# Kernel tuning notes

Hardware: AMD Instinct MI355X
Metric: run time of the kernel (lower is better)

Reference implementation:

```python
import jax, jax.numpy as jnp
import numpy as np

NUM_HEADS = 16
KEY_SIZE = 64
MODEL = NUM_HEADS * KEY_SIZE
B, S = 4, 2048
NEG = jnp.float32(-1e9)


def alibi_bidirectional_bias(num_heads, seq_len):
    # slopes for num_heads//2 heads: 1 / x**(i+1), x = 24**(1/h)
    h = num_heads // 2
    x = 24.0 ** (1.0 / h)
    slopes = (1.0 / x ** jnp.arange(1, h + 1, dtype=jnp.float32))[:, None, None]  # [h,1,1]
    i = jnp.arange(seq_len)
    rel = (i[None, :] - i[:, None]).astype(jnp.float32)  # rel[i,j] = j - i
    # forward (causal): tril(j - i) + (-1e9 strictly above diag)
    fwd = slopes * jnp.tril(rel) + jnp.triu(jnp.full((seq_len, seq_len), NEG), k=1)
    # backward (anti-causal): triu(i - j) + (-1e9 strictly below diag)
    bwd = slopes * jnp.triu(-rel) + jnp.tril(jnp.full((seq_len, seq_len), NEG), k=-1)
    return jnp.concatenate([fwd, bwd], axis=0)  # [num_heads, S, S]


def setup_inputs() -> dict:
    key = jax.random.key(0)
    ks = jax.random.split(key, 11)
    sc = 0.02
    d = {
        "query": jax.random.normal(ks[0], (B, S, MODEL), jnp.float32),
        "key": jax.random.normal(ks[1], (B, S, MODEL), jnp.float32),
        "value": jax.random.normal(ks[2], (B, S, MODEL), jnp.float32),
        "Wq": jax.random.normal(ks[3], (MODEL, MODEL), jnp.float32) * sc,
        "bq": jnp.zeros((MODEL,), jnp.float32),
        "Wk": jax.random.normal(ks[4], (MODEL, MODEL), jnp.float32) * sc,
        "bk": jnp.zeros((MODEL,), jnp.float32),
        "Wv": jax.random.normal(ks[5], (MODEL, MODEL), jnp.float32) * sc,
        "bv": jnp.zeros((MODEL,), jnp.float32),
        "Wo": jax.random.normal(ks[6], (MODEL, MODEL), jnp.float32) * sc,
        "bo": jnp.zeros((MODEL,), jnp.float32),
    }
    return d


def reference(query, key, value, Wq, bq, Wk, bk, Wv, bv, Wo, bo):
    b, s, _ = query.shape
    H, D = NUM_HEADS, KEY_SIZE

    def proj(x, W, bias):
        return (x @ W.T + bias).reshape(b, s, H, D).transpose(0, 2, 1, 3)  # [B,H,S,D]

    q = proj(query, Wq, bq)
    k = proj(key, Wk, bk)
    v = proj(value, Wv, bv)

    bias = alibi_bidirectional_bias(H, s)  # [H,S,S], broadcasts over batch
    scores = jnp.einsum("bhqd,bhkd->bhqk", q, k) / jnp.sqrt(jnp.float32(D)) + bias
    attn = jax.nn.softmax(scores, axis=-1)
    out = jnp.einsum("bhqk,bhkd->bhqd", attn, v)
    out = out.transpose(0, 2, 1, 3).reshape(b, s, H * D)
    return out @ Wo.T + bo
```

## Files before the change

kernel.cpp:

```cpp
#include <hip/hip_runtime.h>
#include <hip/hip_bf16.h>
#include <stdint.h>

typedef unsigned short u16;
typedef __attribute__((ext_vector_type(8))) __bf16 bf16x8;
typedef __attribute__((ext_vector_type(4))) float f32x4;
typedef __attribute__((ext_vector_type(4))) unsigned int u32x4;

#define S_LEN 2048
#define NHEAD 16
#define HDIM 64
#define DMODEL 1024
#define NBATCH 4
#define MTOK (NBATCH * S_LEN)

__device__ __forceinline__ u16 f2bf(float f) {
    uint32_t u = __float_as_uint(f);
    u += 0x7fffu + ((u >> 16) & 1u);
    return (u16)(u >> 16);
}

__device__ __forceinline__ void gld_lds16(const u16* g, u16* l) {
    __builtin_amdgcn_global_load_lds(
        (const __attribute__((address_space(1))) void*)g,
        (__attribute__((address_space(3))) void*)l, 16, 0, 0);
}

__global__ __launch_bounds__(256) void cast_all(
        const float* __restrict__ q, const float* __restrict__ k, const float* __restrict__ v,
        const float* __restrict__ wq, const float* __restrict__ wk,
        const float* __restrict__ wv, const float* __restrict__ wo,
        u16* __restrict__ xq, u16* __restrict__ xk, u16* __restrict__ xv,
        u16* __restrict__ wqb, u16* __restrict__ wkb, u16* __restrict__ wvb,
        u16* __restrict__ wob) {
    size_t idx4 = (size_t)blockIdx.x * 256 + threadIdx.x;
    const float* src;
    u16* dst;
    size_t off;
    if (idx4 < (size_t)3 << 21) {
        int t = (int)(idx4 >> 21);
        off = (idx4 & ((1u << 21) - 1)) * 4;
        src = (t == 0) ? q : (t == 1) ? k : v;
        dst = (t == 0) ? xq : (t == 1) ? xk : xv;
    } else {
        size_t w = idx4 - ((size_t)3 << 21);
        int t = (int)(w >> 18);
        off = (w & ((1u << 18) - 1)) * 4;
        src = (t == 0) ? wq : (t == 1) ? wk : (t == 2) ? wv : wo;
        dst = (t == 0) ? wqb : (t == 1) ? wkb : (t == 2) ? wvb : wob;
    }
    float4 val = *(const float4*)(src + off);
    ushort4 o;
    o.x = f2bf(val.x); o.y = f2bf(val.y); o.z = f2bf(val.z); o.w = f2bf(val.w);
    *(ushort4*)(dst + off) = o;
}

#define TM 128
#define TN 128

__device__ __forceinline__ void gemm_body(const u16* __restrict__ A,
                                          const u16* __restrict__ W,
                                          const float* __restrict__ bias,
                                          void* __restrict__ outp, int mode,
                                          int m0, int n0) {
    __shared__ __align__(16) u16 As[2][TM * 32];
    __shared__ __align__(16) u16 Bs[2][TN * 32];
    const int tid  = threadIdx.x;
    const int lane = tid & 63;
    const int wv   = tid >> 6;
    const int l16  = lane & 15;
    const int quad = lane >> 4;
    const int wm   = (wv >> 1) * 64;
    const int wn   = (wv & 1) * 64;

    f32x4 acc[4][4];
#pragma unroll
    for (int i = 0; i < 4; i++)
#pragma unroll
        for (int j = 0; j < 4; j++) acc[i][j] = {};

    const int arow = wv * 16 + (lane >> 2);
    const int acol = ((lane & 3) ^ ((lane >> 3) & 3)) * 8;
    const u16* gA = A + (size_t)(m0 + arow) * DMODEL + acol;
    const u16* gB = W + (size_t)(n0 + arow) * DMODEL + acol;
    const int loff = wv * 16 * 32;

    const int swz = (l16 >> 1) & 3;

    gld_lds16(gA,                        As[0] + loff);
    gld_lds16(gA + (size_t)64 * DMODEL,  As[0] + loff + 64 * 32);
    gld_lds16(gB,                        Bs[0] + loff);
    gld_lds16(gB + (size_t)64 * DMODEL,  Bs[0] + loff + 64 * 32);

    int buf = 0;
    for (int kb = 0; kb < DMODEL; kb += 32) {
        __builtin_amdgcn_s_waitcnt(0x0F70);
        __syncthreads();
        if (kb + 32 < DMODEL) {
            gld_lds16(gA + kb + 32,                       As[buf ^ 1] + loff);
            gld_lds16(gA + kb + 32 + (size_t)64 * DMODEL, As[buf ^ 1] + loff + 64 * 32);
            gld_lds16(gB + kb + 32,                       Bs[buf ^ 1] + loff);
            gld_lds16(gB + kb + 32 + (size_t)64 * DMODEL, Bs[buf ^ 1] + loff + 64 * 32);
        }

        bf16x8 af[4], bfv[4];
#pragma unroll
        for (int i = 0; i < 4; i++)
            af[i] = *(const bf16x8*)(&As[buf][(wm + i * 16 + l16) * 32 + (quad ^ swz) * 8]);
#pragma unroll
        for (int j = 0; j < 4; j++)
            bfv[j] = *(const bf16x8*)(&Bs[buf][(wn + j * 16 + l16) * 32 + (quad ^ swz) * 8]);
#pragma unroll
        for (int i = 0; i < 4; i++)
#pragma unroll
            for (int j = 0; j < 4; j++)
                acc[i][j] = __builtin_amdgcn_mfma_f32_16x16x32_bf16(af[i], bfv[j], acc[i][j], 0, 0, 0);
        buf ^= 1;
    }

#pragma unroll
    for (int j = 0; j < 4; j++) {
        int n = n0 + wn + j * 16 + l16;
        float bv = bias[n];
#pragma unroll
        for (int i = 0; i < 4; i++) {
            int mbase = m0 + wm + i * 16 + quad * 4;
#pragma unroll
            for (int r = 0; r < 4; r++) {
                int m = mbase + r;
                float v = acc[i][j][r] + bv;
                if (mode == 2) {
                    ((float*)outp)[(size_t)m * DMODEL + n] = v;
                } else {
                    int b = m >> 11, s = m & (S_LEN - 1);
                    int h = n >> 6, d = n & 63;
                    u16* o = (u16*)outp;
                    size_t idx = (mode == 0)
                        ? ((((size_t)(b * NHEAD + h)) * S_LEN + s) * HDIM + d)
                        : ((((size_t)(b * NHEAD + h)) * HDIM + d) * S_LEN + s);
                    o[idx] = f2bf(v);
                }
            }
        }
    }
}

__device__ __forceinline__ void gemm_coords(int& m0, int& n0) {
    const int lid = blockIdx.x + 8 * blockIdx.y;
    const int xcd = lid & 7;
    const int s   = lid >> 3;
    n0 = (s & 7) * TN;
    m0 = ((s >> 3) + 8 * xcd) * TM;
}

__global__ __launch_bounds__(256) void gemm_qkv(
        const u16* __restrict__ xq, const u16* __restrict__ xk, const u16* __restrict__ xv,
        const u16* __restrict__ wq, const u16* __restrict__ wk, const u16* __restrict__ wv,
        const float* __restrict__ bq, const float* __restrict__ bk, const float* __restrict__ bv,
        u16* __restrict__ Qb, u16* __restrict__ Kb, u16* __restrict__ Vb) {
    int z = blockIdx.z;
    const u16* A   = (z == 0) ? xq : (z == 1) ? xk : xv;
    const u16* W   = (z == 0) ? wq : (z == 1) ? wk : wv;
    const float* b = (z == 0) ? bq : (z == 1) ? bk : bv;
    u16* out       = (z == 0) ? Qb : (z == 1) ? Kb : Vb;
    int m0, n0;
    gemm_coords(m0, n0);
    gemm_body(A, W, b, out, (z == 2) ? 1 : 0, m0, n0);
}

__global__ __launch_bounds__(256) void gemm_one(
        const u16* __restrict__ A, const u16* __restrict__ W,
        const float* __restrict__ bias, void* __restrict__ out, int mode) {
    int m0, n0;
    gemm_coords(m0, n0);
    gemm_body(A, W, bias, out, mode, m0, n0);
}

__global__ __launch_bounds__(256, 4) void flash_kernel(
        const u16* __restrict__ Q, const u16* __restrict__ K,
        const u16* __restrict__ Vt, u16* __restrict__ AO) {
    __shared__ __align__(16) u16 Ksm[2][64 * 64];
    __shared__ __align__(16) u16 Vsm[2][64 * 64];
    __shared__ __align__(16) u16 Psm[4][16 * 64];

    const int tid  = threadIdx.x;
    const int wv   = tid >> 6;
    const int lane = tid & 63;
    const int l16  = lane & 15;
    const int quad = lane >> 4;

    const int lid   = blockIdx.x + 16 * blockIdx.y;
    const int xcd   = lid & 7;
    const int slot  = lid >> 3;
    const int bh    = xcd + 8 * (slot >> 4);
    const int g_idx = slot & 15;

    const int h    = bh & (NHEAD - 1);
    const int b    = bh >> 4;
    const bool fwd = (h < 8);
    const int sgn  = fwd ? 1 : -1;
    const float slope2 = __builtin_amdgcn_exp2f(-(float)((h & 7) + 1) * 0.5731203125901445f)
                         * 1.4426950408889634f;
    const float cL = 0.18033688011112042f;

    const u16* Kg = K + (size_t)bh * S_LEN * HDIM;
    const u16* Vg = Vt + (size_t)bh * HDIM * S_LEN;

    const int sr = lane >> 3;
    const int sc = (lane & 7) ^ sr;
    const int r0 = 16 * wv;

    const int cA = quad ^ (l16 & 7);
    const int cB = (quad + 4) ^ (l16 & 7);

    float brt[4][4];
#pragma unroll
    for (int t = 0; t < 4; t++)
#pragma unroll
        for (int r = 0; r < 4; r++)
            brt[t][r] = slope2 * (float)(sgn * (16 * t + l16 - (quad * 4 + r))) - 16.0f;

    int poff[4][4];
#pragma unroll
    for (int r = 0; r < 4; r++) {
        const int prow = quad * 4 + r;
        const int pr7  = prow & 7;
#pragma unroll
        for (int t = 0; t < 4; t++)
            poff[r][t] = prow * 64 + (((2 * t + (l16 >> 3)) ^ pr7) * 8) + (l16 & 7);
    }

    bf16x8 ones;
#pragma unroll
    for (int j = 0; j < 8; j++) ones[j] = (__bf16)1.0f;

    const float dkq = slope2 * (float)(sgn * 64);

#pragma unroll 1
    for (int half = 0; half < 2; half++) {
        const int g  = half ? (31 - g_idx) : g_idx;
        const int q0 = g * 64 + wv * 16;
        const u16* Qp = Q + ((size_t)bh * S_LEN + q0) * HDIM;
        const bf16x8 aq0 = *(const bf16x8*)(Qp + l16 * HDIM + quad * 8);
        const bf16x8 aq1 = *(const bf16x8*)(Qp + l16 * HDIM + 32 + quad * 8);

        f32x4 o[4], osum = {};
#pragma unroll
        for (int dt = 0; dt < 4; dt++) o[dt] = {};

        const int kt0 = fwd ? 0 : g;
        const int kt1 = fwd ? g : (S_LEN / 64 - 1);

        __syncthreads();
        const u16* kg = Kg + ((size_t)(kt0 * 64) + r0 + sr) * 64 + sc * 8;
        const u16* vg = Vg + (size_t)(r0 + sr) * S_LEN + kt0 * 64 + sc * 8;
        gld_lds16(kg,              &Ksm[0][r0 * 64]);
        gld_lds16(kg + 8 * 64,     &Ksm[0][(r0 + 8) * 64]);
        gld_lds16(vg,              &Vsm[0][r0 * 64]);
        gld_lds16(vg + 8 * S_LEN,  &Vsm[0][(r0 + 8) * 64]);
        kg += 64 * 64;
        vg += 64;

        float kq = slope2 * (float)(sgn * (kt0 * 64 - q0));

        int buf = 0;
        for (int kt = kt0; kt <= kt1; ++kt) {
            __builtin_amdgcn_s_waitcnt(0x0F70);
            __syncthreads();
            if (kt < kt1) {
                gld_lds16(kg,             &Ksm[buf ^ 1][r0 * 64]);
                gld_lds16(kg + 8 * 64,    &Ksm[buf ^ 1][(r0 + 8) * 64]);
                gld_lds16(vg,             &Vsm[buf ^ 1][r0 * 64]);
                gld_lds16(vg + 8 * S_LEN, &Vsm[buf ^ 1][(r0 + 8) * 64]);
                kg += 64 * 64;
                vg += 64;
            }
            const u16* Ks = &Ksm[buf][0];
            const u16* Vs = &Vsm[buf][0];

            f32x4 st[4];
#pragma unroll
            for (int t = 0; t < 4; t++) {
                const u16* kp = Ks + (16 * t + l16) * 64;
                bf16x8 k0 = *(const bf16x8*)(kp + cA * 8);
                bf16x8 k1 = *(const bf16x8*)(kp + cB * 8);
                f32x4 c = {};
                c = __builtin_amdgcn_mfma_f32_16x16x32_bf16(aq0, k0, c, 0, 0, 0);
                c = __builtin_amdgcn_mfma_f32_16x16x32_bf16(aq1, k1, c, 0, 0, 0);
                st[t] = c;
            }

            float p[4][4];
            if (kt == g) {
#pragma unroll
                for (int r = 0; r < 4; r++) {
                    const int qg = q0 + quad * 4 + r;
#pragma unroll
                    for (int t = 0; t < 4; t++) {
                        const int kg2 = kt * 64 + 16 * t + l16;
                        const bool ok = fwd ? (kg2 <= qg) : (kg2 >= qg);
                        float s2 = fmaf(st[t][r], cL, brt[t][r] + kq);
                        p[t][r] = ok ? __builtin_amdgcn_exp2f(s2) : 0.0f;
                    }
                }
            } else {
#pragma unroll
                for (int r = 0; r < 4; r++)
#pragma unroll
                    for (int t = 0; t < 4; t++)
                        p[t][r] = __builtin_amdgcn_exp2f(fmaf(st[t][r], cL, brt[t][r] + kq));
            }
            kq += dkq;

            u16* Pw = &Psm[wv][0];
#pragma unroll
            for (int r = 0; r < 4; r++)
#pragma unroll
                for (int t = 0; t < 4; t++)
                    Pw[poff[r][t]] = f2bf(p[t][r]);
            __builtin_amdgcn_s_waitcnt(0xC07F);
            bf16x8 pf0 = *(const bf16x8*)(&Pw[l16 * 64 + cA * 8]);
            bf16x8 pf1 = *(const bf16x8*)(&Pw[l16 * 64 + cB * 8]);

#pragma unroll
            for (int dt = 0; dt < 4; dt++) {
                const u16* vp = Vs + (dt * 16 + l16) * 64;
                bf16x8 v0 = *(const bf16x8*)(vp + cA * 8);
                bf16x8 v1 = *(const bf16x8*)(vp + cB * 8);
                o[dt] = __builtin_amdgcn_mfma_f32_16x16x32_bf16(pf0, v0, o[dt], 0, 0, 0);
                o[dt] = __builtin_amdgcn_mfma_f32_16x16x32_bf16(pf1, v1, o[dt], 0, 0, 0);
            }
            osum = __builtin_amdgcn_mfma_f32_16x16x32_bf16(pf0, ones, osum, 0, 0, 0);
            osum = __builtin_amdgcn_mfma_f32_16x16x32_bf16(pf1, ones, osum, 0, 0, 0);
            buf ^= 1;
        }

#pragma unroll
        for (int r = 0; r < 4; r++) {
            float inv = 1.0f / osum[r];
            int qg = q0 + quad * 4 + r;
            u16* op = AO + ((size_t)b * S_LEN + qg) * DMODEL + h * HDIM;
#pragma unroll
            for (int dt = 0; dt < 4; dt++)
                op[dt * 16 + l16] = f2bf(o[dt][r] * inv);
        }
    }
}

extern "C" void kernel_launch(void* const* d_in, const int* in_sizes, int n_in,
                              void* d_out, int out_size, void* d_ws, size_t ws_size,
                              hipStream_t stream) {
    const float* query = (const float*)d_in[0];
    const float* key   = (const float*)d_in[1];
    const float* value = (const float*)d_in[2];
    const float* Wq    = (const float*)d_in[3];
    const float* bq    = (const float*)d_in[4];
    const float* Wk    = (const float*)d_in[5];
    const float* bk    = (const float*)d_in[6];
    const float* Wv    = (const float*)d_in[7];
    const float* bv    = (const float*)d_in[8];
    const float* Wo    = (const float*)d_in[9];
    const float* bo    = (const float*)d_in[10];

    const size_t Xe = (size_t)MTOK * DMODEL;
    const size_t We = (size_t)DMODEL * DMODEL;
    u16* xq  = (u16*)d_ws;
    u16* xk  = xq + Xe;
    u16* xv  = xk + Xe;
    u16* wqb = xv + Xe;
    u16* wkb = wqb + We;
    u16* wvb = wkb + We;
    u16* wob = wvb + We;
    u16* Qb  = wob + We;
    u16* Kb  = Qb + Xe;
    u16* Vb  = Kb + Xe;
    u16* AO  = Vb + Xe;

    cast_all<<<dim3(28672), dim3(256), 0, stream>>>(
        query, key, value, Wq, Wk, Wv, Wo,
        xq, xk, xv, wqb, wkb, wvb, wob);

    gemm_qkv<<<dim3(DMODEL / TN, MTOK / TM, 3), dim3(256), 0, stream>>>(
        xq, xk, xv, wqb, wkb, wvb, bq, bk, bv, Qb, Kb, Vb);

    flash_kernel<<<dim3(16, NBATCH * NHEAD), dim3(256), 0, stream>>>(Qb, Kb, Vb, AO);

    gemm_one<<<dim3(DMODEL / TN, MTOK / TM, 1), dim3(256), 0, stream>>>(AO, wob, bo, d_out, 2);
}
```

Baseline: 333.9 us.

## Fuse fp32-to-bf16 activation cast into QKV projection GEMM A-tile loads

The separate cast pass over the three fp32 activation tensors is removed. The QKV GEMM now reads fp32 activations directly, converts them to bf16 in registers and writes swizzled tiles into LDS, with global loads for the next k-step overlapped with the MFMAs. This drops a full write and re-read of about 48MB of bf16 intermediates. In exchange, each GEMM block reads twice as many A bytes, and A is re-read across the 8 N-tiles, so the A staging moves from async global-to-LDS to register-staged loads.

```diff
diff --git a/kernel.cpp b/kernel.cpp
--- a/kernel.cpp
+++ b/kernel.cpp
@@ -26,29 +26,25 @@
         (__attribute__((address_space(3))) void*)l, 16, 0, 0);
 }
 
-__global__ __launch_bounds__(256) void cast_all(
-        const float* __restrict__ q, const float* __restrict__ k, const float* __restrict__ v,
+__device__ __forceinline__ void stage8(u16* dst, float4 lo, float4 hi) {
+    __hip_bfloat162 p0 = __float22bfloat162_rn(make_float2(lo.x, lo.y));
+    __hip_bfloat162 p1 = __float22bfloat162_rn(make_float2(lo.z, lo.w));
+    __hip_bfloat162 p2 = __float22bfloat162_rn(make_float2(hi.x, hi.y));
+    __hip_bfloat162 p3 = __float22bfloat162_rn(make_float2(hi.z, hi.w));
+    u32x4 w = { *(uint32_t*)&p0, *(uint32_t*)&p1, *(uint32_t*)&p2, *(uint32_t*)&p3 };
+    *(u32x4*)dst = w;
+}
+
+__global__ __launch_bounds__(256) void cast_w(
         const float* __restrict__ wq, const float* __restrict__ wk,
         const float* __restrict__ wv, const float* __restrict__ wo,
-        u16* __restrict__ xq, u16* __restrict__ xk, u16* __restrict__ xv,
-        u16* __restrict__ wqb, u16* __restrict__ wkb, u16* __restrict__ wvb,
-        u16* __restrict__ wob) {
+        u16* __restrict__ wqb, u16* __restrict__ wkb,
+        u16* __restrict__ wvb, u16* __restrict__ wob) {
     size_t idx4 = (size_t)blockIdx.x * 256 + threadIdx.x;
-    const float* src;
-    u16* dst;
-    size_t off;
-    if (idx4 < (size_t)3 << 21) {
-        int t = (int)(idx4 >> 21);
-        off = (idx4 & ((1u << 21) - 1)) * 4;
-        src = (t == 0) ? q : (t == 1) ? k : v;
-        dst = (t == 0) ? xq : (t == 1) ? xk : xv;
-    } else {
-        size_t w = idx4 - ((size_t)3 << 21);
-        int t = (int)(w >> 18);
-        off = (w & ((1u << 18) - 1)) * 4;
-        src = (t == 0) ? wq : (t == 1) ? wk : (t == 2) ? wv : wo;
-        dst = (t == 0) ? wqb : (t == 1) ? wkb : (t == 2) ? wvb : wob;
-    }
+    int t = (int)(idx4 >> 18);
+    size_t off = (idx4 & ((1u << 18) - 1)) * 4;
+    const float* src = (t == 0) ? wq : (t == 1) ? wk : (t == 2) ? wv : wo;
+    u16* dst         = (t == 0) ? wqb : (t == 1) ? wkb : (t == 2) ? wvb : wob;
     float4 val = *(const float4*)(src + off);
     ushort4 o;
     o.x = f2bf(val.x); o.y = f2bf(val.y); o.z = f2bf(val.z); o.w = f2bf(val.w);
@@ -58,11 +54,19 @@
 #define TM 128
 #define TN 128
 
-__device__ __forceinline__ void gemm_body(const u16* __restrict__ A,
-                                          const u16* __restrict__ W,
-                                          const float* __restrict__ bias,
-                                          void* __restrict__ outp, int mode,
-                                          int m0, int n0) {
+__device__ __forceinline__ void gemm_coords(int& m0, int& n0) {
+    const int lid = blockIdx.x + 8 * blockIdx.y;
+    const int xcd = lid & 7;
+    const int s   = lid >> 3;
+    n0 = (s & 7) * TN;
+    m0 = ((s >> 3) + 8 * xcd) * TM;
+}
+
+__device__ __forceinline__ void gemm_body_f32A(const float* __restrict__ A,
+                                               const u16* __restrict__ W,
+                                               const float* __restrict__ bias,
+                                               u16* __restrict__ outp, int mode,
+                                               int m0, int n0) {
     __shared__ __align__(16) u16 As[2][TM * 32];
     __shared__ __align__(16) u16 Bs[2][TN * 32];
     const int tid  = threadIdx.x;
@@ -79,6 +83,122 @@
 #pragma unroll
         for (int j = 0; j < 4; j++) acc[i][j] = {};
 
+    const int srow = lane >> 2;
+    const int scol = lane & 3;
+    const int sw   = (lane >> 3) & 3;
+    const float* gA = A + (size_t)(m0 + wv * 16 + srow) * DMODEL + scol * 8;
+    const u16*   gB = W + (size_t)(n0 + wv * 16 + srow) * DMODEL + ((scol ^ sw) * 8);
+    const int aoff  = (wv * 16 + srow) * 32 + ((scol ^ sw) * 8);
+    const int boff  = wv * 16 * 32;
+
+    const int swz = (l16 >> 1) & 3;
+
+    {
+        gld_lds16(gB,                       Bs[0] + boff);
+        gld_lds16(gB + (size_t)64 * DMODEL, Bs[0] + boff + 64 * 32);
+        float4 a00 = *(const float4*)(gA);
+        float4 a01 = *(const float4*)(gA + 4);
+        float4 a10 = *(const float4*)(gA + (size_t)64 * DMODEL);
+        float4 a11 = *(const float4*)(gA + (size_t)64 * DMODEL + 4);
+        stage8(&As[0][aoff], a00, a01);
+        stage8(&As[0][aoff + 64 * 32], a10, a11);
+    }
+    __builtin_amdgcn_s_waitcnt(0x0F70);
+    __syncthreads();
+
+    int buf = 0;
+    for (int kb = 0; kb < DMODEL; kb += 32) {
+        const bool next = (kb + 32) < DMODEL;
+        float4 a00, a01, a10, a11;
+        if (next) {
+            gld_lds16(gB + kb + 32,                       Bs[buf ^ 1] + boff);
+            gld_lds16(gB + kb + 32 + (size_t)64 * DMODEL, Bs[buf ^ 1] + boff + 64 * 32);
+            a00 = *(const float4*)(gA + kb + 32);
+            a01 = *(const float4*)(gA + kb + 32 + 4);
+            a10 = *(const float4*)(gA + kb + 32 + (size_t)64 * DMODEL);
+            a11 = *(const float4*)(gA + kb + 32 + (size_t)64 * DMODEL + 4);
+        }
+
+        bf16x8 af[4], bfv[4];
+#pragma unroll
+        for (int i = 0; i < 4; i++)
+            af[i] = *(const bf16x8*)(&As[buf][(wm + i * 16 + l16) * 32 + (quad ^ swz) * 8]);
+#pragma unroll
+        for (int j = 0; j < 4; j++)
+            bfv[j] = *(const bf16x8*)(&Bs[buf][(wn + j * 16 + l16) * 32 + (quad ^ swz) * 8]);
+#pragma unroll
+        for (int i = 0; i < 4; i++)
+#pragma unroll
+            for (int j = 0; j < 4; j++)
+                acc[i][j] = __builtin_amdgcn_mfma_f32_16x16x32_bf16(af[i], bfv[j], acc[i][j], 0, 0, 0);
+
+        if (next) {
+            stage8(&As[buf ^ 1][aoff], a00, a01);
+            stage8(&As[buf ^ 1][aoff + 64 * 32], a10, a11);
+        }
+        __builtin_amdgcn_s_waitcnt(0x0F70);
+        __syncthreads();
+        buf ^= 1;
+    }
+
+#pragma unroll
+    for (int j = 0; j < 4; j++) {
+        int n = n0 + wn + j * 16 + l16;
+        float bv = bias[n];
+#pragma unroll
+        for (int i = 0; i < 4; i++) {
+            int mbase = m0 + wm + i * 16 + quad * 4;
+#pragma unroll
+            for (int r = 0; r < 4; r++) {
+                int m = mbase + r;
+                float v = acc[i][j][r] + bv;
+                int b = m >> 11, s = m & (S_LEN - 1);
+                int h = n >> 6, d = n & 63;
+                size_t idx = (mode == 0)
+                    ? ((((size_t)(b * NHEAD + h)) * S_LEN + s) * HDIM + d)
+                    : ((((size_t)(b * NHEAD + h)) * HDIM + d) * S_LEN + s);
+                outp[idx] = f2bf(v);
+            }
+        }
+    }
+}
+
+__global__ __launch_bounds__(256) void gemm_qkv(
+        const float* __restrict__ xq, const float* __restrict__ xk, const float* __restrict__ xv,
+        const u16* __restrict__ wq, const u16* __restrict__ wk, const u16* __restrict__ wv,
+        const float* __restrict__ bq, const float* __restrict__ bk, const float* __restrict__ bv,
+        u16* __restrict__ Qb, u16* __restrict__ Kb, u16* __restrict__ Vb) {
+    int z = blockIdx.z;
+    const float* A = (z == 0) ? xq : (z == 1) ? xk : xv;
+    const u16* W   = (z == 0) ? wq : (z == 1) ? wk : wv;
+    const float* b = (z == 0) ? bq : (z == 1) ? bk : bv;
+    u16* out       = (z == 0) ? Qb : (z == 1) ? Kb : Vb;
+    int m0, n0;
+    gemm_coords(m0, n0);
+    gemm_body_f32A(A, W, b, out, (z == 2) ? 1 : 0, m0, n0);
+}
+
+__global__ __launch_bounds__(256) void gemm_one(
+        const u16* __restrict__ A, const u16* __restrict__ W,
+        const float* __restrict__ bias, float* __restrict__ out) {
+    __shared__ __align__(16) u16 As[2][TM * 32];
+    __shared__ __align__(16) u16 Bs[2][TN * 32];
+    const int tid  = threadIdx.x;
+    const int lane = tid & 63;
+    const int wv   = tid >> 6;
+    const int l16  = lane & 15;
+    const int quad = lane >> 4;
+    const int wm   = (wv >> 1) * 64;
+    const int wn   = (wv & 1) * 64;
+    int m0, n0;
+    gemm_coords(m0, n0);
+
+    f32x4 acc[4][4];
+#pragma unroll
+    for (int i = 0; i < 4; i++)
+#pragma unroll
+        for (int j = 0; j < 4; j++) acc[i][j] = {};
+
     const int arow = wv * 16 + (lane >> 2);
     const int acol = ((lane & 3) ^ ((lane >> 3) & 3)) * 8;
     const u16* gA = A + (size_t)(m0 + arow) * DMODEL + acol;
@@ -126,54 +246,10 @@
         for (int i = 0; i < 4; i++) {
             int mbase = m0 + wm + i * 16 + quad * 4;
 #pragma unroll
-            for (int r = 0; r < 4; r++) {
-                int m = mbase + r;
-                float v = acc[i][j][r] + bv;
-                if (mode == 2) {
-                    ((float*)outp)[(size_t)m * DMODEL + n] = v;
-                } else {
-                    int b = m >> 11, s = m & (S_LEN - 1);
-                    int h = n >> 6, d = n & 63;
-                    u16* o = (u16*)outp;
-                    size_t idx = (mode == 0)
-                        ? ((((size_t)(b * NHEAD + h)) * S_LEN + s) * HDIM + d)
-                        : ((((size_t)(b * NHEAD + h)) * HDIM + d) * S_LEN + s);
-                    o[idx] = f2bf(v);
-                }
-            }
-        }
-    }
-}
-
-__device__ __forceinline__ void gemm_coords(int& m0, int& n0) {
-    const int lid = blockIdx.x + 8 * blockIdx.y;
-    const int xcd = lid & 7;
-    const int s   = lid >> 3;
-    n0 = (s & 7) * TN;
-    m0 = ((s >> 3) + 8 * xcd) * TM;
-}
-
-__global__ __launch_bounds__(256) void gemm_qkv(
-        const u16* __restrict__ xq, const u16* __restrict__ xk, const u16* __restrict__ xv,
-        const u16* __restrict__ wq, const u16* __restrict__ wk, const u16* __restrict__ wv,
-        const float* __restrict__ bq, const float* __restrict__ bk, const float* __restrict__ bv,
-        u16* __restrict__ Qb, u16* __restrict__ Kb, u16* __restrict__ Vb) {
-    int z = blockIdx.z;
-    const u16* A   = (z == 0) ? xq : (z == 1) ? xk : xv;
-    const u16* W   = (z == 0) ? wq : (z == 1) ? wk : wv;
-    const float* b = (z == 0) ? bq : (z == 1) ? bk : bv;
-    u16* out       = (z == 0) ? Qb : (z == 1) ? Kb : Vb;
-    int m0, n0;
-    gemm_coords(m0, n0);
-    gemm_body(A, W, b, out, (z == 2) ? 1 : 0, m0, n0);
-}
-
-__global__ __launch_bounds__(256) void gemm_one(
-        const u16* __restrict__ A, const u16* __restrict__ W,
-        const float* __restrict__ bias, void* __restrict__ out, int mode) {
-    int m0, n0;
-    gemm_coords(m0, n0);
-    gemm_body(A, W, bias, out, mode, m0, n0);
+            for (int r = 0; r < 4; r++)
+                out[(size_t)(mbase + r) * DMODEL + n] = acc[i][j][r] + bv;
+        }
+    }
 }
 
 __global__ __launch_bounds__(256, 4) void flash_kernel(
@@ -364,10 +440,7 @@
 
     const size_t Xe = (size_t)MTOK * DMODEL;
     const size_t We = (size_t)DMODEL * DMODEL;
-    u16* xq  = (u16*)d_ws;
-    u16* xk  = xq + Xe;
-    u16* xv  = xk + Xe;
-    u16* wqb = xv + Xe;
+    u16* wqb = (u16*)d_ws;
     u16* wkb = wqb + We;
     u16* wvb = wkb + We;
     u16* wob = wvb + We;
@@ -376,14 +449,14 @@
     u16* Vb  = Kb + Xe;
     u16* AO  = Vb + Xe;
 
-    cast_all<<<dim3(28672), dim3(256), 0, stream>>>(
-        query, key, value, Wq, Wk, Wv, Wo,
-        xq, xk, xv, wqb, wkb, wvb, wob);
+    cast_w<<<dim3(4096), dim3(256), 0, stream>>>(
+        Wq, Wk, Wv, Wo, wqb, wkb, wvb, wob);
 
     gemm_qkv<<<dim3(DMODEL / TN, MTOK / TM, 3), dim3(256), 0, stream>>>(
-        xq, xk, xv, wqb, wkb, wvb, bq, bk, bv, Qb, Kb, Vb);
+        query, key, value, wqb, wkb, wvb, bq, bk, bv, Qb, Kb, Vb);
 
     flash_kernel<<<dim3(16, NBATCH * NHEAD), dim3(256), 0, stream>>>(Qb, Kb, Vb, AO);
 
-    gemm_one<<<dim3(DMODEL / TN, MTOK / TM, 1), dim3(256), 0, stream>>>(AO, wob, bo, d_out, 2);
-}
+    gemm_one<<<dim3(DMODEL / TN, MTOK / TM, 1), dim3(256), 0, stream>>>(
+        AO, wob, bo, (float*)d_out);
+}
```

Result: slower. 376.6 us (+12.8%).
